# Kernel tuning notes

Measured on AMD Instinct MI355X. Metric: run time of the kernel, lower is better.

## Reference

```python
import jax, jax.numpy as jnp
import numpy as np

B, T, E, H = 4, 1024, 768, 12
HD = E // H                      # 64
R = 2                            # lora rank
LORA_SCALE = 1.0 / R             # loralib default lora_alpha=1 -> alpha/r
NUM_BUCKETS, MAX_DIST = 320, 800


def _rel_bucket(rel):
    nb = NUM_BUCKETS // 2                      # 160
    buckets = (rel > 0).astype(jnp.int32) * nb
    rel = jnp.abs(rel)
    max_exact = nb // 2                        # 80
    is_small = rel < max_exact
    log_ratio = jnp.log(jnp.maximum(rel, 1).astype(jnp.float32) / max_exact)
    large = max_exact + (log_ratio / np.log(MAX_DIST / max_exact) * (nb - max_exact)).astype(jnp.int32)
    large = jnp.minimum(large, nb - 1)
    return buckets + jnp.where(is_small, rel, large)


def setup_inputs() -> dict:
    key = jax.random.key(0)
    ks = jax.random.split(key, 22)
    s = 0.02
    w = lambda k, shape: jax.random.normal(k, shape, jnp.float32) * s
    return {
        "hidden_states": jax.random.normal(ks[0], (B, T, E), jnp.float32),
        "Wq": w(ks[1], (E, E)), "bq": w(ks[2], (E,)),
        "Wk": w(ks[3], (E, E)), "bk": w(ks[4], (E,)),
        "Wv": w(ks[5], (E, E)), "bv": w(ks[6], (E,)),
        "Aq": w(ks[7], (R, E)), "Bq": w(ks[8], (E, R)),
        "Ak": w(ks[9], (R, E)), "Bk": w(ks[10], (E, R)),
        "Av": w(ks[11], (R, E)), "Bv": w(ks[12], (E, R)),
        "Wo": w(ks[13], (E, E)), "bo": w(ks[14], (E,)),
        "Wg": w(ks[15], (8, HD)), "bg": w(ks[16], (8,)),
        "gru_const": jnp.ones((1, H, 1, 1), jnp.float32),
        "rel_embed": w(ks[17], (NUM_BUCKETS, H)),
    }


def reference(hidden_states, Wq, bq, Wk, bk, Wv, bv,
              Aq, Bq, Ak, Bk, Av, Bv, Wo, bo, Wg, bg, gru_const, rel_embed):
    Bsz, Tq, _ = hidden_states.shape
    # --- relative position bias [H, T, T] ---
    pos = jnp.arange(Tq)
    bucket = _rel_bucket(pos[None, :] - pos[:, None])
    pos_bias = rel_embed[bucket].transpose(2, 0, 1)
    # --- dynamic gate from hidden states, per head/position ---
    g = hidden_states.reshape(Bsz, Tq, H, HD).transpose(0, 2, 1, 3)      # [B,H,T,hd]
    gp = jnp.einsum('bhtd,ed->bhte', g, Wg) + bg                          # [B,H,T,8]
    gp = gp.reshape(Bsz, H, Tq, 2, 4).sum(-1)                             # [B,H,T,2]
    gates = jax.nn.sigmoid(gp)
    gate_a, gate_b = gates[..., :1], gates[..., 1:]
    gate = gate_a * (gate_b * gru_const - 1.0) + 2.0                      # [B,H,T,1]
    gated_bias = gate * pos_bias[None]                                    # [B,H,T,T]
    # --- projections: original double-applies q/k/v_proj (proj+LoRA, then
    #     again inside F.multi_head_attention_forward via separate proj weights) ---
    lin = lambda x, W, b: jnp.einsum('bte,oe->bto', x, W) + b
    lora = lambda x, A, Bm: jnp.einsum('bte,re,or->bto', x, A, Bm) * LORA_SCALE
    x = hidden_states
    q1 = lin(x, Wq, bq) + lora(x, Aq, Bq)
    k1 = lin(x, Wk, bk) + lora(x, Ak, Bk)
    v1 = lin(x, Wv, bv) + lora(x, Av, Bv)
    q = lin(q1, Wq, bq) * (HD ** -0.5)
    k = lin(k1, Wk, bk)
    v = lin(v1, Wv, bv)
    qh = q.reshape(Bsz, Tq, H, HD).transpose(0, 2, 1, 3)
    kh = k.reshape(Bsz, Tq, H, HD).transpose(0, 2, 1, 3)
    vh = v.reshape(Bsz, Tq, H, HD).transpose(0, 2, 1, 3)
    scores = jnp.einsum('bhqd,bhkd->bhqk', qh, kh) + gated_bias
    attn = jax.nn.softmax(scores, axis=-1)
    ctx = jnp.einsum('bhqk,bhkd->bhqd', attn, vh)
    out = ctx.transpose(0, 2, 1, 3).reshape(Bsz, Tq, E)
    return jnp.einsum('bte,oe->bto', out, Wo) + bo
```

## Files before the change

kernel.cpp:

```cpp
#include <hip/hip_runtime.h>
#include <math.h>

#define TT 1024
#define EE 768
#define HH 12

typedef __attribute__((ext_vector_type(8))) __bf16 bf16x8;
typedef __attribute__((ext_vector_type(4))) float f32x4;

__device__ __forceinline__ unsigned short f2b(float f) {
    unsigned int u = __float_as_uint(f);
    unsigned int r = (u + 0x7fffu + ((u >> 16) & 1u)) >> 16;
    return (unsigned short)r;
}

#define GLD16(gsrc, ldst) \
    __builtin_amdgcn_global_load_lds( \
        (const __attribute__((address_space(1))) unsigned int*)(gsrc), \
        (__attribute__((address_space(3))) unsigned int*)(ldst), 16, 0, 0)

__global__ __launch_bounds__(256)
void setupA_k(const float* __restrict__ Wq, const float* __restrict__ Wk,
              const float* __restrict__ Wv, const float* __restrict__ Wo,
              const float* __restrict__ bq, const float* __restrict__ bk,
              const float* __restrict__ bv,
              const float* __restrict__ Bq, const float* __restrict__ Bk,
              const float* __restrict__ Bv, const float* __restrict__ rel,
              unsigned short* __restrict__ Wall_b, unsigned short* __restrict__ WT_all,
              float* __restrict__ biasTab, float* __restrict__ bias2,
              float* __restrict__ B2) {
    __shared__ __align__(16) char smem[34816];
    const int bid = blockIdx.x, tid = threadIdx.x;

    if (bid < 1152) {
        size_t base = (size_t)bid * 2048 + tid * 8;
        int mat = (int)(base / 589824);
        size_t local = base % 589824;
        const float* S = mat == 0 ? Wq : (mat == 1 ? Wk : (mat == 2 ? Wv : Wo));
        float4 a = *(const float4*)&S[local];
        float4 c = *(const float4*)&S[local + 4];
        unsigned short hb[8] __attribute__((aligned(16)));
        hb[0] = f2b(a.x); hb[1] = f2b(a.y); hb[2] = f2b(a.z); hb[3] = f2b(a.w);
        hb[4] = f2b(c.x); hb[5] = f2b(c.y); hb[6] = f2b(c.z); hb[7] = f2b(c.w);
        *(uint4*)&Wall_b[base] = *(const uint4*)hb;
    } else if (bid < 1260) {
        unsigned short* Ts = (unsigned short*)smem;
        int v = bid - 1152;
        int mat = v / 36, tile = v % 36;
        int tr = tile / 6, tc = tile % 6;
        const float* S = mat == 0 ? Wq : (mat == 1 ? Wk : Wv);
        #pragma unroll
        for (int i = 0; i < 16; ++i) {
            int idx = i * 256 + tid;
            int row = idx >> 5, col4 = (idx & 31) * 4;
            float4 f = *(const float4*)&S[(size_t)(tr * 128 + row) * EE + tc * 128 + col4];
            Ts[(col4 + 0) * 136 + row] = f2b(f.x);
            Ts[(col4 + 1) * 136 + row] = f2b(f.y);
            Ts[(col4 + 2) * 136 + row] = f2b(f.z);
            Ts[(col4 + 3) * 136 + row] = f2b(f.w);
        }
        __syncthreads();
        unsigned short* dst = WT_all + (size_t)mat * 589824;
        #pragma unroll
        for (int i = 0; i < 8; ++i) {
            int idx = i * 256 + tid;
            int rr = idx >> 4, cg = (idx & 15) * 8;
            *(uint4*)&dst[(size_t)(tc * 128 + rr) * EE + tr * 128 + cg] =
                *(const uint4*)&Ts[rr * 136 + cg];
        }
    } else if (bid < 1356) {
        int idx = (bid - 1260) * 256 + tid;
        if (idx < 2047 * 12) {
            int h = idx % 12;
            int rr = idx / 12;
            int relv = rr - 1023;
            int base = relv > 0 ? 160 : 0;
            int ar = relv < 0 ? -relv : relv;
            int bkt;
            if (ar < 80) bkt = base + ar;
            else {
                double lr = log((double)ar / 80.0);
                int large = 80 + (int)(lr / log(10.0) * 80.0);
                if (large > 159) large = 159;
                bkt = base + large;
            }
            biasTab[h * 2048 + rr] = rel[bkt * 12 + h];
        }
    } else {
        float* bvS = (float*)smem;
        float* BmS = bvS + 768;
        int v = bid - 1356;
        int sel = v / 4, nb = (v % 4) * 192;
        const float* W = sel == 0 ? Wq : (sel == 1 ? Wk : Wv);
        const float* bvec = sel == 0 ? bq : (sel == 1 ? bk : bv);
        const float* Bm = sel == 0 ? Bq : (sel == 1 ? Bk : Bv);
        for (int i = tid; i < 768; i += 256) bvS[i] = bvec[i];
        for (int i = tid; i < 1536; i += 256) BmS[i] = Bm[i];
        __syncthreads();
        if (tid < 192) {
            int n = nb + tid;
            const float* Wrow = W + (size_t)n * EE;
            float a0 = 0.f, a1 = 0.f, a2 = 0.f;
            for (int o = 0; o < EE; o += 4) {
                float4 w = *(const float4*)&Wrow[o];
                a0 += w.x * bvS[o] + w.y * bvS[o + 1] + w.z * bvS[o + 2] + w.w * bvS[o + 3];
                a1 += w.x * BmS[o * 2] + w.y * BmS[o * 2 + 2] + w.z * BmS[o * 2 + 4] + w.w * BmS[o * 2 + 6];
                a2 += w.x * BmS[o * 2 + 1] + w.y * BmS[o * 2 + 3] + w.z * BmS[o * 2 + 5] + w.w * BmS[o * 2 + 7];
            }
            float sc = (sel == 0) ? 0.125f : 1.0f;
            bias2[sel * 768 + n] = (a0 + bvS[n]) * sc;
            B2[sel * 1536 + n * 2 + 0] = a1 * sc;
            B2[sel * 1536 + n * 2 + 1] = a2 * sc;
        }
    }
}

__global__ __launch_bounds__(256)
void setupB_k(const float* __restrict__ hs, const float* __restrict__ Wg,
              const float* __restrict__ bg, const float* __restrict__ gru,
              const float* __restrict__ Aq, const float* __restrict__ Ak,
              const float* __restrict__ Av,
              unsigned short* __restrict__ hsb, float* __restrict__ gate,
              float* __restrict__ xA) {
    __shared__ float rowF[16 * 772];
    __shared__ float AS[6 * 768];
    __shared__ float WgS[8 * 68];
    __shared__ float gpS[16 * 100];
    __shared__ float redS[4 * 96];
    __shared__ float bgS[8];
    __shared__ float gcS[12];
    const int tid = threadIdx.x;
    const int m0 = blockIdx.x * 16;

    for (int i = tid; i < 512; i += 256) WgS[(i >> 6) * 68 + (i & 63)] = Wg[i];
    for (int i = tid; i < 1152; i += 256) {
        int which = i / 192, c4 = (i % 192) * 4;
        const float* src = (which < 2 ? Aq : (which < 4 ? Ak : Av)) + (which & 1) * 768 + c4;
        float4 f = *(const float4*)src;
        AS[which * 768 + c4 + 0] = f.x; AS[which * 768 + c4 + 1] = f.y;
        AS[which * 768 + c4 + 2] = f.z; AS[which * 768 + c4 + 3] = f.w;
    }
    if (tid < 8)  bgS[tid] = bg[tid];
    if (tid < 12) gcS[tid] = gru[tid];
    #pragma unroll
    for (int i = 0; i < 12; ++i) {
        int idx = i * 256 + tid;
        int row = idx / 192, c4 = (idx % 192) * 4;
        float4 f = *(const float4*)&hs[(size_t)(m0 + row) * EE + c4];
        rowF[row * 772 + c4 + 0] = f.x; rowF[row * 772 + c4 + 1] = f.y;
        rowF[row * 772 + c4 + 2] = f.z; rowF[row * 772 + c4 + 3] = f.w;
        unsigned int lo = (unsigned int)f2b(f.x) | ((unsigned int)f2b(f.y) << 16);
        unsigned int hi = (unsigned int)f2b(f.z) | ((unsigned int)f2b(f.w) << 16);
        uint2 p; p.x = lo; p.y = hi;
        *(uint2*)&hsb[(size_t)(m0 + row) * EE + c4] = p;
    }
    __syncthreads();
    #pragma unroll
    for (int j = 0; j < 6; ++j) {
        int idx = j * 256 + tid;
        int row = idx & 15, q = idx >> 4;
        int h = q % 12, e = q / 12;
        const float* rp = &rowF[row * 772 + h * 64];
        const float* wp = &WgS[e * 68];
        float a = 0.f;
        #pragma unroll 16
        for (int d = 0; d < 64; ++d) a += rp[d] * wp[d];
        gpS[row * 100 + h * 8 + e] = a;
    }
    {
        int row = tid & 15, seg = tid >> 4;
        float s[6] = {0.f, 0.f, 0.f, 0.f, 0.f, 0.f};
        #pragma unroll 8
        for (int j = 0; j < 48; ++j) {
            int e = seg * 48 + j;
            float xv = rowF[row * 772 + e];
            s[0] += xv * AS[e];            s[1] += xv * AS[768 + e];
            s[2] += xv * AS[1536 + e];     s[3] += xv * AS[2304 + e];
            s[4] += xv * AS[3072 + e];     s[5] += xv * AS[3840 + e];
        }
        #pragma unroll
        for (int i = 0; i < 6; ++i) {
            s[i] += __shfl_xor(s[i], 16, 64);
            s[i] += __shfl_xor(s[i], 32, 64);
        }
        int lane = tid & 63, w = tid >> 6;
        if ((lane >> 4) == 0)
            #pragma unroll
            for (int i = 0; i < 6; ++i) redS[w * 96 + row * 6 + i] = s[i];
    }
    __syncthreads();
    if (tid < 96) {
        int row = tid / 6, i = tid % 6;
        float v = redS[row * 6 + i] + redS[96 + row * 6 + i] +
                  redS[192 + row * 6 + i] + redS[288 + row * 6 + i];
        int sel = i >> 1, r = i & 1;
        xA[sel * 8192 + (size_t)(m0 + row) * 2 + r] = v;
    }
    if (tid < 192) {
        int row = tid / 12, h = tid % 12;
        const float* gp = &gpS[row * 100 + h * 8];
        float s0 = gp[0] + gp[1] + gp[2] + gp[3] + bgS[0] + bgS[1] + bgS[2] + bgS[3];
        float s1 = gp[4] + gp[5] + gp[6] + gp[7] + bgS[4] + bgS[5] + bgS[6] + bgS[7];
        float ga = 1.f / (1.f + __expf(-s0));
        float gb = 1.f / (1.f + __expf(-s1));
        int m = m0 + row;
        int b = m >> 10, tp = m & 1023;
        gate[((size_t)b * HH + h) * TT + tp] = ga * (gb * gcS[h] - 1.0f) + 2.0f;
    }
}

__global__ __launch_bounds__(256, 3)
void wgemm_k(const unsigned short* __restrict__ Wall_b,
             const unsigned short* __restrict__ WT_all,
             unsigned short* __restrict__ W2_all) {
    __shared__ unsigned short At[128 * 32];
    __shared__ unsigned short Bt[128 * 32];
    const int tid = threadIdx.x;
    const int bxx = blockIdx.x;
    const int sel = bxx / 36, tile = bxx % 36;
    const int row0 = (tile / 6) * 128, col0 = (tile % 6) * 128;
    const unsigned short* A = Wall_b + (size_t)sel * 589824;
    const unsigned short* Bw = WT_all + (size_t)sel * 589824;

    const int lane = tid & 63, wv = tid >> 6;
    const int wm = (wv & 1) * 64, wn = (wv >> 1) * 64;
    const int l15 = lane & 15, g8 = (lane >> 4) * 8;
    const int lr = lane >> 2, lc = (lane & 3) * 8;
    const int c0 = wv * 2, c1 = wv * 2 + 1;
    const unsigned short* Abase0 = A + (size_t)(row0 + c0 * 16 + lr) * EE + lc;
    const unsigned short* Abase1 = A + (size_t)(row0 + c1 * 16 + lr) * EE + lc;
    const unsigned short* Bbase0 = Bw + (size_t)(col0 + c0 * 16 + lr) * EE + lc;
    const unsigned short* Bbase1 = Bw + (size_t)(col0 + c1 * 16 + lr) * EE + lc;

    f32x4 zero4 = {0.f, 0.f, 0.f, 0.f};
    f32x4 acc[4][4];
    #pragma unroll
    for (int i = 0; i < 4; ++i)
        #pragma unroll
        for (int j = 0; j < 4; ++j) acc[i][j] = zero4;

    for (int kt = 0; kt < 768; kt += 32) {
        GLD16(Abase0 + kt, &At[c0 * 512]);
        GLD16(Abase1 + kt, &At[c1 * 512]);
        GLD16(Bbase0 + kt, &Bt[c0 * 512]);
        GLD16(Bbase1 + kt, &Bt[c1 * 512]);
        __syncthreads();
        bf16x8 af[4], bf[4];
        #pragma unroll
        for (int mt = 0; mt < 4; ++mt) af[mt] = *(const bf16x8*)&At[(wm + mt * 16 + l15) * 32 + g8];
        #pragma unroll
        for (int nt = 0; nt < 4; ++nt) bf[nt] = *(const bf16x8*)&Bt[(wn + nt * 16 + l15) * 32 + g8];
        #pragma unroll
        for (int mt = 0; mt < 4; ++mt)
            #pragma unroll
            for (int nt = 0; nt < 4; ++nt)
                acc[mt][nt] = __builtin_amdgcn_mfma_f32_16x16x32_bf16(af[mt], bf[nt], acc[mt][nt], 0, 0, 0);
        __syncthreads();
    }
    unsigned short* out = W2_all + (size_t)sel * 589824;
    const float sc = (sel == 0) ? 0.125f : 1.0f;
    const int g4 = (lane >> 4) * 4;
    #pragma unroll
    for (int mt = 0; mt < 4; ++mt)
        #pragma unroll
        for (int r = 0; r < 4; ++r) {
            int grow = row0 + wm + mt * 16 + g4 + r;
            #pragma unroll
            for (int nt = 0; nt < 4; ++nt) {
                int ncol = col0 + wn + nt * 16 + l15;
                out[(size_t)grow * EE + ncol] = f2b(acc[mt][nt][r] * sc);
            }
        }
}

__global__ __launch_bounds__(256, 3)
void qkv_gemm_k(const unsigned short* __restrict__ Aall,
                const unsigned short* __restrict__ W2_all,
                const float* __restrict__ bias2,
                const float* __restrict__ xA, const float* __restrict__ B2,
                unsigned short* __restrict__ qb, unsigned short* __restrict__ kb,
                unsigned short* __restrict__ vb) {
    __shared__ unsigned short At[128 * 32];
    __shared__ unsigned short Bt[128 * 32];
    const int tid = threadIdx.x;
    const int bx = blockIdx.x, by = blockIdx.y;
    const int sel = bx / 6;
    const int col0 = (bx % 6) * 128, row0 = by * 128;
    const unsigned short* Wb = W2_all + (size_t)sel * 589824;
    const float* bias = bias2 + sel * 768;

    const int lane = tid & 63, wv = tid >> 6;
    const int wm = (wv & 1) * 64, wn = (wv >> 1) * 64;
    const int l15 = lane & 15, g8 = (lane >> 4) * 8;
    const int lr = lane >> 2, lc = (lane & 3) * 8;
    const int c0 = wv * 2, c1 = wv * 2 + 1;
    const unsigned short* Abase0 = Aall + (size_t)(row0 + c0 * 16 + lr) * EE + lc;
    const unsigned short* Abase1 = Aall + (size_t)(row0 + c1 * 16 + lr) * EE + lc;
    const unsigned short* Bbase0 = Wb + (size_t)(col0 + c0 * 16 + lr) * EE + lc;
    const unsigned short* Bbase1 = Wb + (size_t)(col0 + c1 * 16 + lr) * EE + lc;

    f32x4 zero4 = {0.f, 0.f, 0.f, 0.f};
    f32x4 acc[4][4];
    #pragma unroll
    for (int i = 0; i < 4; ++i)
        #pragma unroll
        for (int j = 0; j < 4; ++j) acc[i][j] = zero4;

    for (int kt = 0; kt < 768; kt += 32) {
        GLD16(Abase0 + kt, &At[c0 * 512]);
        GLD16(Abase1 + kt, &At[c1 * 512]);
        GLD16(Bbase0 + kt, &Bt[c0 * 512]);
        GLD16(Bbase1 + kt, &Bt[c1 * 512]);
        __syncthreads();
        bf16x8 af[4], bf[4];
        #pragma unroll
        for (int mt = 0; mt < 4; ++mt) af[mt] = *(const bf16x8*)&At[(wm + mt * 16 + l15) * 32 + g8];
        #pragma unroll
        for (int nt = 0; nt < 4; ++nt) bf[nt] = *(const bf16x8*)&Bt[(wn + nt * 16 + l15) * 32 + g8];
        #pragma unroll
        for (int mt = 0; mt < 4; ++mt)
            #pragma unroll
            for (int nt = 0; nt < 4; ++nt)
                acc[mt][nt] = __builtin_amdgcn_mfma_f32_16x16x32_bf16(af[mt], bf[nt], acc[mt][nt], 0, 0, 0);
        __syncthreads();
    }

    unsigned short* dst = sel == 0 ? qb : (sel == 1 ? kb : vb);
    const float* Lbase = xA + sel * 8192;
    const float* B2s   = B2 + sel * 1536;
    const int g4 = (lane >> 4) * 4;
    #pragma unroll
    for (int mt = 0; mt < 4; ++mt) {
        #pragma unroll
        for (int r = 0; r < 4; ++r) {
            size_t grow = (size_t)row0 + wm + mt * 16 + g4 + r;
            float l0 = Lbase[grow * 2], l1 = Lbase[grow * 2 + 1];
            #pragma unroll
            for (int nt = 0; nt < 4; ++nt) {
                int ncol = col0 + wn + nt * 16 + l15;
                float c = acc[mt][nt][r] + bias[ncol]
                          + 0.5f * (l0 * B2s[ncol * 2] + l1 * B2s[ncol * 2 + 1]);
                dst[grow * EE + ncol] = f2b(c);
            }
        }
    }
}

__global__ __launch_bounds__(256)
void vT_k(const unsigned short* __restrict__ vb, unsigned short* __restrict__ Vtg) {
    __shared__ unsigned short Vs[64 * 72];
    const int tid = threadIdx.x;
    const int tt = blockIdx.x, h = blockIdx.y, b = blockIdx.z;
    const int r = tid >> 3, cc = (tid & 7) * 8;
    #pragma unroll
    for (int i = 0; i < 2; ++i) {
        int row = i * 32 + r;
        const unsigned short* vp = vb + (size_t)(b * TT + tt * 64 + row) * EE + h * 64 + cc;
        *(uint4*)&Vs[row * 72 + cc] = *(const uint4*)vp;
    }
    __syncthreads();
    #pragma unroll
    for (int i = 0; i < 2; ++i) {
        int d = i * 32 + r;
        unsigned short tmp[8] __attribute__((aligned(16)));
        #pragma unroll
        for (int j = 0; j < 8; ++j) tmp[j] = Vs[(cc + j) * 72 + d];
        *(uint4*)&Vtg[((size_t)(b * HH + h) * 64 + d) * TT + tt * 64 + cc] = *(const uint4*)tmp;
    }
}

__global__ __launch_bounds__(256, 3)
void attn_k(const unsigned short* __restrict__ qb, const unsigned short* __restrict__ kb,
            const unsigned short* __restrict__ Vtg, const float* __restrict__ gate,
            const float* __restrict__ biasTab, unsigned short* __restrict__ ctx) {
    __shared__ unsigned short Qs[64 * 72];
    __shared__ unsigned short Ks[64 * 72];
    __shared__ unsigned short Vt[64 * 72];
    __shared__ unsigned short Ps[64 * 72];
    __shared__ float btabS[2048];
    const int tid = threadIdx.x;
    const int qt = blockIdx.x, h = blockIdx.y, b = blockIdx.z;

    for (int i = tid; i < 2047; i += 256) btabS[i] = biasTab[h * 2048 + i];

    const int srow = tid >> 2, scol = (tid & 3) * 16;
    {
        const unsigned short* qp = qb + ((size_t)(b * TT + qt * 64 + srow)) * EE + h * 64 + scol;
        *(uint4*)&Qs[srow * 72 + scol]     = *(const uint4*)qp;
        *(uint4*)&Qs[srow * 72 + scol + 8] = *(const uint4*)(qp + 8);
    }
    const int lane = tid & 63, wv = tid >> 6;
    const int m0 = wv * 16;
    const int l15 = lane & 15, g = lane >> 4;

    float li[4];
    f32x4 zero4 = {0.f, 0.f, 0.f, 0.f};
    f32x4 oa[4];
    #pragma unroll
    for (int r = 0; r < 4; ++r) li[r] = 0.f;
    #pragma unroll
    for (int nt = 0; nt < 4; ++nt) oa[nt] = zero4;
    float gv[4];
    #pragma unroll
    for (int r = 0; r < 4; ++r)
        gv[r] = gate[((size_t)(b * HH + h)) * TT + qt * 64 + m0 + 4 * g + r];

    const unsigned short* kpbase = kb + ((size_t)(b * TT + srow)) * EE + h * 64 + scol;
    const unsigned short* vpbase = Vtg + ((size_t)(b * HH + h) * 64 + srow) * TT + scol;

    uint4 kr0 = *(const uint4*)kpbase;
    uint4 kr1 = *(const uint4*)(kpbase + 8);
    uint4 vr0 = *(const uint4*)vpbase;
    uint4 vr1 = *(const uint4*)(vpbase + 8);

    for (int kt = 0; kt < 16; ++kt) {
        __syncthreads();
        *(uint4*)&Ks[srow * 72 + scol]     = kr0;
        *(uint4*)&Ks[srow * 72 + scol + 8] = kr1;
        *(uint4*)&Vt[srow * 72 + scol]     = vr0;
        *(uint4*)&Vt[srow * 72 + scol + 8] = vr1;
        __syncthreads();
        if (kt < 15) {
            const unsigned short* kp = kpbase + (size_t)(kt + 1) * 64 * EE;
            kr0 = *(const uint4*)kp;
            kr1 = *(const uint4*)(kp + 8);
            const unsigned short* vp = vpbase + (kt + 1) * 64;
            vr0 = *(const uint4*)vp;
            vr1 = *(const uint4*)(vp + 8);
        }
        f32x4 sa[4];
        #pragma unroll
        for (int nt = 0; nt < 4; ++nt) sa[nt] = zero4;
        bf16x8 aq0 = *(const bf16x8*)&Qs[(m0 + l15) * 72 + g * 8];
        bf16x8 aq1 = *(const bf16x8*)&Qs[(m0 + l15) * 72 + 32 + g * 8];
        #pragma unroll
        for (int nt = 0; nt < 4; ++nt) {
            bf16x8 bk0 = *(const bf16x8*)&Ks[(nt * 16 + l15) * 72 + g * 8];
            bf16x8 bk1 = *(const bf16x8*)&Ks[(nt * 16 + l15) * 72 + 32 + g * 8];
            sa[nt] = __builtin_amdgcn_mfma_f32_16x16x32_bf16(aq0, bk0, sa[nt], 0, 0, 0);
            sa[nt] = __builtin_amdgcn_mfma_f32_16x16x32_bf16(aq1, bk1, sa[nt], 0, 0, 0);
        }
        #pragma unroll
        for (int nt = 0; nt < 4; ++nt) {
            int ibase = kt * 64 + nt * 16 + l15 + 1023 - qt * 64 - m0 - 4 * g;
            #pragma unroll
            for (int r = 0; r < 4; ++r) {
                float e = __expf(sa[nt][r] + gv[r] * btabS[ibase - r]);
                li[r] += e;
                Ps[(m0 + 4 * g + r) * 72 + nt * 16 + l15] = f2b(e);
            }
        }
        bf16x8 ap0 = *(const bf16x8*)&Ps[(m0 + l15) * 72 + g * 8];
        bf16x8 ap1 = *(const bf16x8*)&Ps[(m0 + l15) * 72 + 32 + g * 8];
        #pragma unroll
        for (int nt = 0; nt < 4; ++nt) {
            bf16x8 bv0 = *(const bf16x8*)&Vt[(nt * 16 + l15) * 72 + g * 8];
            bf16x8 bv1 = *(const bf16x8*)&Vt[(nt * 16 + l15) * 72 + 32 + g * 8];
            oa[nt] = __builtin_amdgcn_mfma_f32_16x16x32_bf16(ap0, bv0, oa[nt], 0, 0, 0);
            oa[nt] = __builtin_amdgcn_mfma_f32_16x16x32_bf16(ap1, bv1, oa[nt], 0, 0, 0);
        }
    }
    __syncthreads();
    #pragma unroll
    for (int r = 0; r < 4; ++r) {
        #pragma unroll
        for (int msk = 1; msk < 16; msk <<= 1)
            li[r] += __shfl_xor(li[r], msk, 16);
    }
    #pragma unroll
    for (int nt = 0; nt < 4; ++nt)
        #pragma unroll
        for (int r = 0; r < 4; ++r)
            Ks[(m0 + 4 * g + r) * 72 + nt * 16 + l15] = f2b(oa[nt][r] / li[r]);
    __syncthreads();
    {
        unsigned short* cp = ctx + ((size_t)(b * TT + qt * 64 + srow)) * EE + h * 64 + scol;
        *(uint4*)cp       = *(const uint4*)&Ks[srow * 72 + scol];
        *(uint4*)(cp + 8) = *(const uint4*)&Ks[srow * 72 + scol + 8];
    }
}

__global__ __launch_bounds__(256, 3)
void out_gemm_k(const unsigned short* __restrict__ Aall,
                const unsigned short* __restrict__ Wob,
                const float* __restrict__ bo, float* __restrict__ outf) {
    __shared__ unsigned short At[128 * 32];
    __shared__ unsigned short Bt[128 * 32];
    const int tid = threadIdx.x;
    const int col0 = blockIdx.x * 128, row0 = blockIdx.y * 128;

    const int lane = tid & 63, wv = tid >> 6;
    const int wm = (wv & 1) * 64, wn = (wv >> 1) * 64;
    const int l15 = lane & 15, g8 = (lane >> 4) * 8;
    const int lr = lane >> 2, lc = (lane & 3) * 8;
    const int c0 = wv * 2, c1 = wv * 2 + 1;
    const unsigned short* Abase0 = Aall + (size_t)(row0 + c0 * 16 + lr) * EE + lc;
    const unsigned short* Abase1 = Aall + (size_t)(row0 + c1 * 16 + lr) * EE + lc;
    const unsigned short* Bbase0 = Wob + (size_t)(col0 + c0 * 16 + lr) * EE + lc;
    const unsigned short* Bbase1 = Wob + (size_t)(col0 + c1 * 16 + lr) * EE + lc;

    f32x4 zero4 = {0.f, 0.f, 0.f, 0.f};
    f32x4 acc[4][4];
    #pragma unroll
    for (int i = 0; i < 4; ++i)
        #pragma unroll
        for (int j = 0; j < 4; ++j) acc[i][j] = zero4;

    for (int kt = 0; kt < 768; kt += 32) {
        GLD16(Abase0 + kt, &At[c0 * 512]);
        GLD16(Abase1 + kt, &At[c1 * 512]);
        GLD16(Bbase0 + kt, &Bt[c0 * 512]);
        GLD16(Bbase1 + kt, &Bt[c1 * 512]);
        __syncthreads();
        bf16x8 af[4], bf[4];
        #pragma unroll
        for (int mt = 0; mt < 4; ++mt) af[mt] = *(const bf16x8*)&At[(wm + mt * 16 + l15) * 32 + g8];
        #pragma unroll
        for (int nt = 0; nt < 4; ++nt) bf[nt] = *(const bf16x8*)&Bt[(wn + nt * 16 + l15) * 32 + g8];
        #pragma unroll
        for (int mt = 0; mt < 4; ++mt)
            #pragma unroll
            for (int nt = 0; nt < 4; ++nt)
                acc[mt][nt] = __builtin_amdgcn_mfma_f32_16x16x32_bf16(af[mt], bf[nt], acc[mt][nt], 0, 0, 0);
        __syncthreads();
    }
    const int g4 = (lane >> 4) * 4;
    #pragma unroll
    for (int mt = 0; mt < 4; ++mt)
        #pragma unroll
        for (int r = 0; r < 4; ++r) {
            size_t grow = (size_t)row0 + wm + mt * 16 + g4 + r;
            #pragma unroll
            for (int nt = 0; nt < 4; ++nt) {
                int ncol = col0 + wn + nt * 16 + l15;
                outf[grow * EE + ncol] = acc[mt][nt][r] + bo[ncol];
            }
        }
}

extern "C" void kernel_launch(void* const* d_in, const int* in_sizes, int n_in,
                              void* d_out, int out_size, void* d_ws, size_t ws_size,
                              hipStream_t stream) {
    const float* hs  = (const float*)d_in[0];
    const float* Wq  = (const float*)d_in[1];
    const float* bq  = (const float*)d_in[2];
    const float* Wk  = (const float*)d_in[3];
    const float* bk  = (const float*)d_in[4];
    const float* Wv  = (const float*)d_in[5];
    const float* bv  = (const float*)d_in[6];
    const float* Aq  = (const float*)d_in[7];
    const float* Bq  = (const float*)d_in[8];
    const float* Ak  = (const float*)d_in[9];
    const float* Bk  = (const float*)d_in[10];
    const float* Av  = (const float*)d_in[11];
    const float* Bv  = (const float*)d_in[12];
    const float* Wo  = (const float*)d_in[13];
    const float* bo  = (const float*)d_in[14];
    const float* Wg  = (const float*)d_in[15];
    const float* bg  = (const float*)d_in[16];
    const float* gru = (const float*)d_in[17];
    const float* rel = (const float*)d_in[18];

    float* ws = (float*)d_ws;
    float* gate    = ws;
    float* biasTab = gate + 49152;
    float* xA      = biasTab + 24576;
    float* bias2   = xA + 24576;
    float* B2      = bias2 + 2304;
    unsigned short* hsb    = (unsigned short*)(B2 + 4608);
    unsigned short* Wall_b = hsb + 3145728;
    unsigned short* WT_all = Wall_b + 4 * 589824;
    unsigned short* W2_all = WT_all + 3 * 589824;
    unsigned short* qb     = W2_all + 3 * 589824;
    unsigned short* kb     = qb + 3145728;
    unsigned short* vb     = kb + 3145728;
    unsigned short* Vtg    = vb + 3145728;
    unsigned short* ctxb   = Vtg + 3145728;

    setupA_k<<<1368, 256, 0, stream>>>(Wq, Wk, Wv, Wo, bq, bk, bv, Bq, Bk, Bv, rel,
                                       Wall_b, WT_all, biasTab, bias2, B2);
    setupB_k<<<256, 256, 0, stream>>>(hs, Wg, bg, gru, Aq, Ak, Av, hsb, gate, xA);
    wgemm_k<<<108, 256, 0, stream>>>(Wall_b, WT_all, W2_all);
    qkv_gemm_k<<<dim3(18, 32), 256, 0, stream>>>(hsb, W2_all, bias2, xA, B2, qb, kb, vb);
    vT_k<<<dim3(16, 12, 4), 256, 0, stream>>>(vb, Vtg);
    attn_k<<<dim3(16, 12, 4), 256, 0, stream>>>(qb, kb, Vtg, gate, biasTab, ctxb);
    out_gemm_k<<<dim3(6, 32), 256, 0, stream>>>(ctxb, Wall_b + 3 * 589824, bo, (float*)d_out);
}
```

Measured before the change: 248.3 us.

## Merge setup kernels, read attention bias from global, shrink output GEMM tile

Merges the two setup kernels into one launch by dispatching on block index, which removes a kernel launch and lets the two kinds of work overlap. The attention kernel no longer stages the per-head bias table in shared memory; it reads it from global/cache with an fmaf, and its launch bound rises to 4 blocks per SM. The output GEMM uses 64-row tiles instead of 128, doubling the grid for better CU fill, also with a 4-block launch bound. The risks are that the merged setup block now needs about 78 KB of shared memory, which limits its occupancy, and that the uncached bias loads add global-memory latency inside the softmax loop.

```diff
diff --git a/kernel.cpp b/kernel.cpp
--- a/kernel.cpp
+++ b/kernel.cpp
@@ -20,16 +20,23 @@
         (__attribute__((address_space(3))) unsigned int*)(ldst), 16, 0, 0)
 
 __global__ __launch_bounds__(256)
-void setupA_k(const float* __restrict__ Wq, const float* __restrict__ Wk,
-              const float* __restrict__ Wv, const float* __restrict__ Wo,
-              const float* __restrict__ bq, const float* __restrict__ bk,
-              const float* __restrict__ bv,
-              const float* __restrict__ Bq, const float* __restrict__ Bk,
-              const float* __restrict__ Bv, const float* __restrict__ rel,
-              unsigned short* __restrict__ Wall_b, unsigned short* __restrict__ WT_all,
-              float* __restrict__ biasTab, float* __restrict__ bias2,
-              float* __restrict__ B2) {
-    __shared__ __align__(16) char smem[34816];
+void setup_k(const float* __restrict__ hs,
+             const float* __restrict__ Wq, const float* __restrict__ Wk,
+             const float* __restrict__ Wv, const float* __restrict__ Wo,
+             const float* __restrict__ bq, const float* __restrict__ bk,
+             const float* __restrict__ bv,
+             const float* __restrict__ Aq, const float* __restrict__ Ak,
+             const float* __restrict__ Av,
+             const float* __restrict__ Bq, const float* __restrict__ Bk,
+             const float* __restrict__ Bv,
+             const float* __restrict__ Wg, const float* __restrict__ bg,
+             const float* __restrict__ gru, const float* __restrict__ rel,
+             unsigned short* __restrict__ Wall_b, unsigned short* __restrict__ WT_all,
+             float* __restrict__ biasTab, float* __restrict__ bias2,
+             float* __restrict__ B2,
+             unsigned short* __restrict__ hsb, float* __restrict__ gate,
+             float* __restrict__ xA) {
+    __shared__ __align__(16) char smem[78080];
     const int bid = blockIdx.x, tid = threadIdx.x;
 
     if (bid < 1152) {
@@ -86,7 +93,7 @@
             }
             biasTab[h * 2048 + rr] = rel[bkt * 12 + h];
         }
-    } else {
+    } else if (bid < 1368) {
         float* bvS = (float*)smem;
         float* BmS = bvS + 768;
         int v = bid - 1356;
@@ -112,100 +119,91 @@
             B2[sel * 1536 + n * 2 + 0] = a1 * sc;
             B2[sel * 1536 + n * 2 + 1] = a2 * sc;
         }
-    }
-}
-
-__global__ __launch_bounds__(256)
-void setupB_k(const float* __restrict__ hs, const float* __restrict__ Wg,
-              const float* __restrict__ bg, const float* __restrict__ gru,
-              const float* __restrict__ Aq, const float* __restrict__ Ak,
-              const float* __restrict__ Av,
-              unsigned short* __restrict__ hsb, float* __restrict__ gate,
-              float* __restrict__ xA) {
-    __shared__ float rowF[16 * 772];
-    __shared__ float AS[6 * 768];
-    __shared__ float WgS[8 * 68];
-    __shared__ float gpS[16 * 100];
-    __shared__ float redS[4 * 96];
-    __shared__ float bgS[8];
-    __shared__ float gcS[12];
-    const int tid = threadIdx.x;
-    const int m0 = blockIdx.x * 16;
-
-    for (int i = tid; i < 512; i += 256) WgS[(i >> 6) * 68 + (i & 63)] = Wg[i];
-    for (int i = tid; i < 1152; i += 256) {
-        int which = i / 192, c4 = (i % 192) * 4;
-        const float* src = (which < 2 ? Aq : (which < 4 ? Ak : Av)) + (which & 1) * 768 + c4;
-        float4 f = *(const float4*)src;
-        AS[which * 768 + c4 + 0] = f.x; AS[which * 768 + c4 + 1] = f.y;
-        AS[which * 768 + c4 + 2] = f.z; AS[which * 768 + c4 + 3] = f.w;
-    }
-    if (tid < 8)  bgS[tid] = bg[tid];
-    if (tid < 12) gcS[tid] = gru[tid];
-    #pragma unroll
-    for (int i = 0; i < 12; ++i) {
-        int idx = i * 256 + tid;
-        int row = idx / 192, c4 = (idx % 192) * 4;
-        float4 f = *(const float4*)&hs[(size_t)(m0 + row) * EE + c4];
-        rowF[row * 772 + c4 + 0] = f.x; rowF[row * 772 + c4 + 1] = f.y;
-        rowF[row * 772 + c4 + 2] = f.z; rowF[row * 772 + c4 + 3] = f.w;
-        unsigned int lo = (unsigned int)f2b(f.x) | ((unsigned int)f2b(f.y) << 16);
-        unsigned int hi = (unsigned int)f2b(f.z) | ((unsigned int)f2b(f.w) << 16);
-        uint2 p; p.x = lo; p.y = hi;
-        *(uint2*)&hsb[(size_t)(m0 + row) * EE + c4] = p;
-    }
-    __syncthreads();
-    #pragma unroll
-    for (int j = 0; j < 6; ++j) {
-        int idx = j * 256 + tid;
-        int row = idx & 15, q = idx >> 4;
-        int h = q % 12, e = q / 12;
-        const float* rp = &rowF[row * 772 + h * 64];
-        const float* wp = &WgS[e * 68];
-        float a = 0.f;
-        #pragma unroll 16
-        for (int d = 0; d < 64; ++d) a += rp[d] * wp[d];
-        gpS[row * 100 + h * 8 + e] = a;
-    }
-    {
-        int row = tid & 15, seg = tid >> 4;
-        float s[6] = {0.f, 0.f, 0.f, 0.f, 0.f, 0.f};
-        #pragma unroll 8
-        for (int j = 0; j < 48; ++j) {
-            int e = seg * 48 + j;
-            float xv = rowF[row * 772 + e];
-            s[0] += xv * AS[e];            s[1] += xv * AS[768 + e];
-            s[2] += xv * AS[1536 + e];     s[3] += xv * AS[2304 + e];
-            s[4] += xv * AS[3072 + e];     s[5] += xv * AS[3840 + e];
-        }
-        #pragma unroll
-        for (int i = 0; i < 6; ++i) {
-            s[i] += __shfl_xor(s[i], 16, 64);
-            s[i] += __shfl_xor(s[i], 32, 64);
-        }
-        int lane = tid & 63, w = tid >> 6;
-        if ((lane >> 4) == 0)
-            #pragma unroll
-            for (int i = 0; i < 6; ++i) redS[w * 96 + row * 6 + i] = s[i];
-    }
-    __syncthreads();
-    if (tid < 96) {
-        int row = tid / 6, i = tid % 6;
-        float v = redS[row * 6 + i] + redS[96 + row * 6 + i] +
-                  redS[192 + row * 6 + i] + redS[288 + row * 6 + i];
-        int sel = i >> 1, r = i & 1;
-        xA[sel * 8192 + (size_t)(m0 + row) * 2 + r] = v;
-    }
-    if (tid < 192) {
-        int row = tid / 12, h = tid % 12;
-        const float* gp = &gpS[row * 100 + h * 8];
-        float s0 = gp[0] + gp[1] + gp[2] + gp[3] + bgS[0] + bgS[1] + bgS[2] + bgS[3];
-        float s1 = gp[4] + gp[5] + gp[6] + gp[7] + bgS[4] + bgS[5] + bgS[6] + bgS[7];
-        float ga = 1.f / (1.f + __expf(-s0));
-        float gb = 1.f / (1.f + __expf(-s1));
-        int m = m0 + row;
-        int b = m >> 10, tp = m & 1023;
-        gate[((size_t)b * HH + h) * TT + tp] = ga * (gb * gcS[h] - 1.0f) + 2.0f;
+    } else {
+        float* rowF = (float*)smem;
+        float* AS   = rowF + 16 * 772;
+        float* WgS  = AS + 6 * 768;
+        float* gpS  = WgS + 8 * 68;
+        float* redS = gpS + 16 * 100;
+        float* bgS  = redS + 4 * 96;
+        float* gcS  = bgS + 8;
+        const int m0 = (bid - 1368) * 16;
+
+        for (int i = tid; i < 512; i += 256) WgS[(i >> 6) * 68 + (i & 63)] = Wg[i];
+        for (int i = tid; i < 1152; i += 256) {
+            int which = i / 192, c4 = (i % 192) * 4;
+            const float* src = (which < 2 ? Aq : (which < 4 ? Ak : Av)) + (which & 1) * 768 + c4;
+            float4 f = *(const float4*)src;
+            AS[which * 768 + c4 + 0] = f.x; AS[which * 768 + c4 + 1] = f.y;
+            AS[which * 768 + c4 + 2] = f.z; AS[which * 768 + c4 + 3] = f.w;
+        }
+        if (tid < 8)  bgS[tid] = bg[tid];
+        if (tid < 12) gcS[tid] = gru[tid];
+        #pragma unroll
+        for (int i = 0; i < 12; ++i) {
+            int idx = i * 256 + tid;
+            int row = idx / 192, c4 = (idx % 192) * 4;
+            float4 f = *(const float4*)&hs[(size_t)(m0 + row) * EE + c4];
+            rowF[row * 772 + c4 + 0] = f.x; rowF[row * 772 + c4 + 1] = f.y;
+            rowF[row * 772 + c4 + 2] = f.z; rowF[row * 772 + c4 + 3] = f.w;
+            unsigned int lo = (unsigned int)f2b(f.x) | ((unsigned int)f2b(f.y) << 16);
+            unsigned int hi = (unsigned int)f2b(f.z) | ((unsigned int)f2b(f.w) << 16);
+            uint2 p; p.x = lo; p.y = hi;
+            *(uint2*)&hsb[(size_t)(m0 + row) * EE + c4] = p;
+        }
+        __syncthreads();
+        #pragma unroll
+        for (int j = 0; j < 6; ++j) {
+            int idx = j * 256 + tid;
+            int row = idx & 15, q = idx >> 4;
+            int h = q % 12, e = q / 12;
+            const float* rp = &rowF[row * 772 + h * 64];
+            const float* wp = &WgS[e * 68];
+            float a = 0.f;
+            #pragma unroll 16
+            for (int d = 0; d < 64; ++d) a += rp[d] * wp[d];
+            gpS[row * 100 + h * 8 + e] = a;
+        }
+        {
+            int row = tid & 15, seg = tid >> 4;
+            float s[6] = {0.f, 0.f, 0.f, 0.f, 0.f, 0.f};
+            #pragma unroll 8
+            for (int j = 0; j < 48; ++j) {
+                int e = seg * 48 + j;
+                float xv = rowF[row * 772 + e];
+                s[0] += xv * AS[e];            s[1] += xv * AS[768 + e];
+                s[2] += xv * AS[1536 + e];     s[3] += xv * AS[2304 + e];
+                s[4] += xv * AS[3072 + e];     s[5] += xv * AS[3840 + e];
+            }
+            #pragma unroll
+            for (int i = 0; i < 6; ++i) {
+                s[i] += __shfl_xor(s[i], 16, 64);
+                s[i] += __shfl_xor(s[i], 32, 64);
+            }
+            int lane = tid & 63, w = tid >> 6;
+            if ((lane >> 4) == 0)
+                #pragma unroll
+                for (int i = 0; i < 6; ++i) redS[w * 96 + row * 6 + i] = s[i];
+        }
+        __syncthreads();
+        if (tid < 96) {
+            int row = tid / 6, i = tid % 6;
+            float v = redS[row * 6 + i] + redS[96 + row * 6 + i] +
+                      redS[192 + row * 6 + i] + redS[288 + row * 6 + i];
+            int sel = i >> 1, r = i & 1;
+            xA[sel * 8192 + (size_t)(m0 + row) * 2 + r] = v;
+        }
+        if (tid < 192) {
+            int row = tid / 12, h = tid % 12;
+            const float* gp = &gpS[row * 100 + h * 8];
+            float s0 = gp[0] + gp[1] + gp[2] + gp[3] + bgS[0] + bgS[1] + bgS[2] + bgS[3];
+            float s1 = gp[4] + gp[5] + gp[6] + gp[7] + bgS[4] + bgS[5] + bgS[6] + bgS[7];
+            float ga = 1.f / (1.f + __expf(-s0));
+            float gb = 1.f / (1.f + __expf(-s1));
+            int m = m0 + row;
+            int b = m >> 10, tp = m & 1023;
+            gate[((size_t)b * HH + h) * TT + tp] = ga * (gb * gcS[h] - 1.0f) + 2.0f;
+        }
     }
 }
 
@@ -369,7 +367,7 @@
     }
 }
 
-__global__ __launch_bounds__(256, 3)
+__global__ __launch_bounds__(256, 4)
 void attn_k(const unsigned short* __restrict__ qb, const unsigned short* __restrict__ kb,
             const unsigned short* __restrict__ Vtg, const float* __restrict__ gate,
             const float* __restrict__ biasTab, unsigned short* __restrict__ ctx) {
@@ -377,11 +375,8 @@
     __shared__ unsigned short Ks[64 * 72];
     __shared__ unsigned short Vt[64 * 72];
     __shared__ unsigned short Ps[64 * 72];
-    __shared__ float btabS[2048];
     const int tid = threadIdx.x;
     const int qt = blockIdx.x, h = blockIdx.y, b = blockIdx.z;
-
-    for (int i = tid; i < 2047; i += 256) btabS[i] = biasTab[h * 2048 + i];
 
     const int srow = tid >> 2, scol = (tid & 3) * 16;
     {
@@ -407,6 +402,7 @@
 
     const unsigned short* kpbase = kb + ((size_t)(b * TT + srow)) * EE + h * 64 + scol;
     const unsigned short* vpbase = Vtg + ((size_t)(b * HH + h) * 64 + srow) * TT + scol;
+    const float* btab = biasTab + h * 2048 + 1023 + l15 - qt * 64 - m0 - 4 * g;
 
     uint4 kr0 = *(const uint4*)kpbase;
     uint4 kr1 = *(const uint4*)(kpbase + 8);
@@ -442,10 +438,10 @@
         }
         #pragma unroll
         for (int nt = 0; nt < 4; ++nt) {
-            int ibase = kt * 64 + nt * 16 + l15 + 1023 - qt * 64 - m0 - 4 * g;
+            const float* bt = btab + kt * 64 + nt * 16;
             #pragma unroll
             for (int r = 0; r < 4; ++r) {
-                float e = __expf(sa[nt][r] + gv[r] * btabS[ibase - r]);
+                float e = __expf(fmaf(gv[r], bt[-r], sa[nt][r]));
                 li[r] += e;
                 Ps[(m0 + 4 * g + r) * 72 + nt * 16 + l15] = f2b(e);
             }
@@ -480,45 +476,43 @@
     }
 }
 
-__global__ __launch_bounds__(256, 3)
+__global__ __launch_bounds__(256, 4)
 void out_gemm_k(const unsigned short* __restrict__ Aall,
                 const unsigned short* __restrict__ Wob,
                 const float* __restrict__ bo, float* __restrict__ outf) {
-    __shared__ unsigned short At[128 * 32];
+    __shared__ unsigned short At[64 * 32];
     __shared__ unsigned short Bt[128 * 32];
     const int tid = threadIdx.x;
-    const int col0 = blockIdx.x * 128, row0 = blockIdx.y * 128;
+    const int col0 = blockIdx.x * 128, row0 = blockIdx.y * 64;
 
     const int lane = tid & 63, wv = tid >> 6;
-    const int wm = (wv & 1) * 64, wn = (wv >> 1) * 64;
+    const int wm = (wv & 1) * 32, wn = (wv >> 1) * 64;
     const int l15 = lane & 15, g8 = (lane >> 4) * 8;
     const int lr = lane >> 2, lc = (lane & 3) * 8;
     const int c0 = wv * 2, c1 = wv * 2 + 1;
-    const unsigned short* Abase0 = Aall + (size_t)(row0 + c0 * 16 + lr) * EE + lc;
-    const unsigned short* Abase1 = Aall + (size_t)(row0 + c1 * 16 + lr) * EE + lc;
+    const unsigned short* Abase  = Aall + (size_t)(row0 + wv * 16 + lr) * EE + lc;
     const unsigned short* Bbase0 = Wob + (size_t)(col0 + c0 * 16 + lr) * EE + lc;
     const unsigned short* Bbase1 = Wob + (size_t)(col0 + c1 * 16 + lr) * EE + lc;
 
     f32x4 zero4 = {0.f, 0.f, 0.f, 0.f};
-    f32x4 acc[4][4];
-    #pragma unroll
-    for (int i = 0; i < 4; ++i)
+    f32x4 acc[2][4];
+    #pragma unroll
+    for (int i = 0; i < 2; ++i)
         #pragma unroll
         for (int j = 0; j < 4; ++j) acc[i][j] = zero4;
 
     for (int kt = 0; kt < 768; kt += 32) {
-        GLD16(Abase0 + kt, &At[c0 * 512]);
-        GLD16(Abase1 + kt, &At[c1 * 512]);
+        GLD16(Abase + kt, &At[wv * 512]);
         GLD16(Bbase0 + kt, &Bt[c0 * 512]);
         GLD16(Bbase1 + kt, &Bt[c1 * 512]);
         __syncthreads();
-        bf16x8 af[4], bf[4];
-        #pragma unroll
-        for (int mt = 0; mt < 4; ++mt) af[mt] = *(const bf16x8*)&At[(wm + mt * 16 + l15) * 32 + g8];
+        bf16x8 af[2], bf[4];
+        #pragma unroll
+        for (int mt = 0; mt < 2; ++mt) af[mt] = *(const bf16x8*)&At[(wm + mt * 16 + l15) * 32 + g8];
         #pragma unroll
         for (int nt = 0; nt < 4; ++nt) bf[nt] = *(const bf16x8*)&Bt[(wn + nt * 16 + l15) * 32 + g8];
         #pragma unroll
-        for (int mt = 0; mt < 4; ++mt)
+        for (int mt = 0; mt < 2; ++mt)
             #pragma unroll
             for (int nt = 0; nt < 4; ++nt)
                 acc[mt][nt] = __builtin_amdgcn_mfma_f32_16x16x32_bf16(af[mt], bf[nt], acc[mt][nt], 0, 0, 0);
@@ -526,7 +520,7 @@
     }
     const int g4 = (lane >> 4) * 4;
     #pragma unroll
-    for (int mt = 0; mt < 4; ++mt)
+    for (int mt = 0; mt < 2; ++mt)
         #pragma unroll
         for (int r = 0; r < 4; ++r) {
             size_t grow = (size_t)row0 + wm + mt * 16 + g4 + r;
@@ -577,12 +571,13 @@
     unsigned short* Vtg    = vb + 3145728;
     unsigned short* ctxb   = Vtg + 3145728;
 
-    setupA_k<<<1368, 256, 0, stream>>>(Wq, Wk, Wv, Wo, bq, bk, bv, Bq, Bk, Bv, rel,
-                                       Wall_b, WT_all, biasTab, bias2, B2);
-    setupB_k<<<256, 256, 0, stream>>>(hs, Wg, bg, gru, Aq, Ak, Av, hsb, gate, xA);
+    setup_k<<<1624, 256, 0, stream>>>(hs, Wq, Wk, Wv, Wo, bq, bk, bv,
+                                      Aq, Ak, Av, Bq, Bk, Bv, Wg, bg, gru, rel,
+                                      Wall_b, WT_all, biasTab, bias2, B2,
+                                      hsb, gate, xA);
     wgemm_k<<<108, 256, 0, stream>>>(Wall_b, WT_all, W2_all);
     qkv_gemm_k<<<dim3(18, 32), 256, 0, stream>>>(hsb, W2_all, bias2, xA, B2, qb, kb, vb);
     vT_k<<<dim3(16, 12, 4), 256, 0, stream>>>(vb, Vtg);
     attn_k<<<dim3(16, 12, 4), 256, 0, stream>>>(qb, kb, Vtg, gate, biasTab, ctxb);
-    out_gemm_k<<<dim3(6, 32), 256, 0, stream>>>(ctxb, Wall_b + 3 * 589824, bo, (float*)d_out);
-}
+    out_gemm_k<<<dim3(6, 64), 256, 0, stream>>>(ctxb, Wall_b + 3 * 589824, bo, (float*)d_out);
+}
```

Measured after the change: 230.7 us. 1.08x faster.
